# Performance work log

Hardware: AMD Instinct MI355X
Metric: run time of the kernel (lower is better)

The kernel has to match this reference:

```python
import jax, jax.numpy as jnp
import numpy as np

G = 32      # num_groups
T = 5       # Newton-Schulz iterations
EPS = 1e-5


def setup_inputs() -> dict:
    key = jax.random.key(0)
    x = jax.random.normal(key, (64, 256, 56, 56), dtype=jnp.float32)
    weight = jnp.ones((1, 256, 1, 1), dtype=jnp.float32)
    bias = jnp.zeros((1, 256, 1, 1), dtype=jnp.float32)
    return {"x": x, "weight": weight, "bias": bias}


def reference(x, weight, bias):
    N, C, H, W = x.shape
    # group view: (N*C//G, G, H, W) -> (G, N*C//G, H, W) -> (G, m)
    xg = x.reshape(N * C // G, G, H, W)
    xg = jnp.transpose(xg, (1, 0, 2, 3)).reshape(G, -1)
    m = xg.shape[1]

    mean = jnp.mean(xg, axis=1, keepdims=True)           # (G, 1)
    xm = xg - mean                                       # (G, m)
    sigma = (xm @ xm.T) / m + EPS * jnp.eye(G, dtype=x.dtype)  # (G, G)

    trace_inv = 1.0 / jnp.trace(sigma)
    sigma_N = sigma * trace_inv

    # Newton-Schulz: P_{k+1} = 1.5*P_k - 0.5*P_k^3 @ sigma_N
    P = jnp.eye(G, dtype=x.dtype)
    for _ in range(T):
        P = 1.5 * P - 0.5 * (P @ P @ P) @ sigma_N
    wm = P * jnp.sqrt(trace_inv)                         # inverse sqrt of sigma

    y = wm @ xm                                          # (G, m)
    out = y.reshape(G, N * C // G, H, W)
    out = jnp.transpose(out, (1, 0, 2, 3)).reshape(N, C, H, W)
    return out * weight + bias
```

## Files before the change

kernel.cpp:

```cpp
#include <hip/hip_runtime.h>


#define EPS 1e-5f
#define NS_ITERS 5
#define HW_ 3136
#define PANELS 512
#define PANEL_STRIDE 100352
#define M_COLS 1605632.0f
#define TPP 49
#define TILES_TOTAL 25088
#define NB1 512

#define WS_GRAM 0
#define WS_SUM 1024
#define WS_WMT 1056
#define WS_SHIFT 2080

typedef __attribute__((ext_vector_type(4))) float f32x4;
typedef __attribute__((ext_vector_type(8))) short short8v;

__device__ __forceinline__ unsigned f2bf2(float a, float b) {
  unsigned ua = __float_as_uint(a); ua = (ua + 0x7FFFu + ((ua >> 16) & 1u)) >> 16;
  unsigned ub = __float_as_uint(b); ub = (ub + 0x7FFFu + ((ub >> 16) & 1u)) >> 16;
  return ua | (ub << 16);
}

__device__ __forceinline__ int swzbyte(int r, int slotq) {
  const int ph = (((slotq) ^ (r & 7)) + 2 * (r >> 3)) & 7;
  return r * 128 + ph * 16;
}

__global__ __launch_bounds__(256) void k_stats(const float* __restrict__ x,
                                               float* __restrict__ ws) {
  __shared__ __align__(16) float smem[2048];
  unsigned short* tile = (unsigned short*)smem;
  const int tid = threadIdx.x;
  const int row_w = tid >> 4;
  const int c4 = tid & 15;
  const int pos = c4 << 2;
  const int wv = tid >> 6;
  const int lane = tid & 63;

  const int wa_lo = swzbyte(row_w, pos >> 3) + (pos & 7) * 2;
  const int wa_hi = swzbyte(row_w + 16, pos >> 3) + (pos & 7) * 2;

  const int fr_r = lane & 15;
  const int fr_sq = (wv >> 1) * 4 + (lane >> 4);
  const int ra0 = swzbyte(fr_r, fr_sq);
  const int ra1 = swzbyte(fr_r + 16, fr_sq);
  const bool bsel = (wv & 1);

  f32x4 acc0 = {0.f, 0.f, 0.f, 0.f};
  f32x4 acc1 = {0.f, 0.f, 0.f, 0.f};
  float sum_lo = 0.f, sum_hi = 0.f;

  for (int t = blockIdx.x; t < TILES_TOTAL; t += gridDim.x) {
    const int panel = t / TPP;
    const int tin = t - panel * TPP;
    const unsigned base = (unsigned)panel * PANEL_STRIDE + ((unsigned)tin << 6);
    const float4 v0 = *(const float4*)(x + base + row_w * HW_ + pos);
    const float4 v1 = *(const float4*)(x + base + (row_w + 16) * HW_ + pos);
    __syncthreads();
    *(uint2*)((char*)tile + wa_lo) = make_uint2(f2bf2(v0.x, v0.y), f2bf2(v0.z, v0.w));
    *(uint2*)((char*)tile + wa_hi) = make_uint2(f2bf2(v1.x, v1.y), f2bf2(v1.z, v1.w));
    sum_lo += v0.x + v0.y + v0.z + v0.w;
    sum_hi += v1.x + v1.y + v1.z + v1.w;
    __syncthreads();
    const short8v f0 = *(const short8v*)((char*)tile + ra0);
    const short8v f1 = *(const short8v*)((char*)tile + ra1);
    const short8v fB = bsel ? f1 : f0;
    acc0 = __builtin_amdgcn_mfma_f32_16x16x32_bf16(f0, fB, acc0, 0, 0, 0);
    acc1 = __builtin_amdgcn_mfma_f32_16x16x32_bf16(f1, fB, acc1, 0, 0, 0);
  }

  __syncthreads();
  {
    float* dst = smem + wv * 512 + lane * 8;
#pragma unroll
    for (int r = 0; r < 4; ++r) { dst[r] = acc0[r]; dst[4 + r] = acc1[r]; }
  }
  __syncthreads();
#pragma unroll
  for (int q = 0; q < 4; ++q) {
    const int e = q * 256 + tid;
    const int R = e >> 5, C = e & 31;
    const int cbh = C >> 4;
    const int ln = (((R & 15) >> 2) << 4) | (C & 15);
    const int idx = ((R >> 4) << 2) | (R & 3);
    const float s = smem[cbh * 512 + ln * 8 + idx] + smem[(cbh + 2) * 512 + ln * 8 + idx];
    atomicAdd(ws + WS_GRAM + e, s);
  }

  __syncthreads();
  smem[tid] = sum_lo;
  smem[256 + tid] = sum_hi;
  __syncthreads();
  if (tid < 32) {
    const int base2 = (tid < 16) ? tid * 16 : 256 + (tid - 16) * 16;
    float s = 0.f;
#pragma unroll
    for (int k = 0; k < 16; ++k) s += smem[base2 + k];
    atomicAdd(ws + WS_SUM + tid, s);
  }
}

__device__ __forceinline__ void mm32(float* __restrict__ D, const float* __restrict__ A,
                                     const float* __restrict__ B, int i, int cbase) {
  f32x4 a0 = {0.f,0.f,0.f,0.f}, a1 = a0, a2 = a0, a3 = a0;
#pragma unroll
  for (int k = 0; k < 32; ++k) {
    const float av = A[i * 36 + k];
    const float4 b0 = *(const float4*)(B + k * 36 + cbase);
    const float4 b1 = *(const float4*)(B + k * 36 + cbase + 4);
    const float4 b2 = *(const float4*)(B + k * 36 + cbase + 8);
    const float4 b3 = *(const float4*)(B + k * 36 + cbase + 12);
    a0[0] += av * b0.x; a0[1] += av * b0.y; a0[2] += av * b0.z; a0[3] += av * b0.w;
    a1[0] += av * b1.x; a1[1] += av * b1.y; a1[2] += av * b1.z; a1[3] += av * b1.w;
    a2[0] += av * b2.x; a2[1] += av * b2.y; a2[2] += av * b2.z; a2[3] += av * b2.w;
    a3[0] += av * b3.x; a3[1] += av * b3.y; a3[2] += av * b3.z; a3[3] += av * b3.w;
  }
  float* d = D + i * 36 + cbase;
#pragma unroll
  for (int r = 0; r < 4; ++r) { d[r] = a0[r]; d[4 + r] = a1[r]; d[8 + r] = a2[r]; d[12 + r] = a3[r]; }
}

__global__ __launch_bounds__(64) void k_ns(float* __restrict__ ws,
                                           const float* __restrict__ weight,
                                           const float* __restrict__ bias) {
  __shared__ float P[32 * 36], S[32 * 36], T1[32 * 36], T2[32 * 36];
  __shared__ float mean[32], msv[64], misc[1];
  const int lane = threadIdx.x;
  const int i = lane & 31;
  const int cbase = (lane >> 5) * 16;
  const float inv_m = 1.0f / M_COLS;

  if (lane < 32) mean[lane] = ws[WS_SUM + lane] * inv_m;
  __syncthreads();
#pragma unroll
  for (int q = 0; q < 16; ++q) {
    const int e = q * 64 + lane;
    const int R = e >> 5, C = e & 31;
    S[R * 36 + C] = ws[WS_GRAM + e] * inv_m - mean[R] * mean[C] + ((R == C) ? EPS : 0.f);
  }
  __syncthreads();
  if (lane == 0) {
    float tr = 0.f;
#pragma unroll
    for (int k = 0; k < 32; ++k) tr += S[k * 36 + k];
    misc[0] = 1.0f / tr;
  }
  __syncthreads();
  const float tinv = misc[0];
#pragma unroll
  for (int q = 0; q < 16; ++q) {
    const int e = q * 64 + lane;
    const int R = e >> 5, C = e & 31;
    S[R * 36 + C] *= tinv;
    P[R * 36 + C] = (R == C) ? 1.f : 0.f;
  }
  __syncthreads();

  for (int it = 0; it < NS_ITERS; ++it) {
    mm32(T1, P, P, i, cbase);
    __syncthreads();
    mm32(T2, T1, P, i, cbase);
    __syncthreads();
    mm32(T1, T2, S, i, cbase);
    __syncthreads();
#pragma unroll
    for (int cc = 0; cc < 16; ++cc) {
      const int c = cbase + cc;
      P[i * 36 + c] = 1.5f * P[i * 36 + c] - 0.5f * T1[i * 36 + c];
    }
    __syncthreads();
  }

  const float sq = sqrtf(tinv);
  float part = 0.f;
#pragma unroll
  for (int cc = 0; cc < 16; ++cc) {
    const int c = cbase + cc;
    const float wmv = P[i * 36 + c] * sq;
    ws[WS_WMT + c * 32 + i] = wmv;
    part += wmv * mean[c];
  }
  msv[lane] = part;
  __syncthreads();
#pragma unroll
  for (int q = 0; q < 4; ++q) {
    const int c = q * 64 + lane;
    const float m2 = msv[c & 31] + msv[32 + (c & 31)];
    ws[WS_SHIFT + c] = bias[c] - weight[c] * m2;
  }
}

__global__ __launch_bounds__(256, 4) void k_apply(const float* __restrict__ x,
                                                  const float* __restrict__ weight,
                                                  const float* __restrict__ ws,
                                                  float* __restrict__ out) {
  __shared__ float wmT[1024];
  __shared__ float wt[256], sh[256];
  const int tid = threadIdx.x;
  *(float4*)(wmT + tid * 4) = *(const float4*)(ws + WS_WMT + tid * 4);
  wt[tid] = weight[tid];
  sh[tid] = ws[WS_SHIFT + tid];
  __syncthreads();

  const unsigned J = blockIdx.x * 512u + (unsigned)tid * 2u;
  const unsigned panel = J / HW_;
  const unsigned p = J - panel * HW_;
  const unsigned base = panel * PANEL_STRIDE + p;
  const int cb = (int)(panel & 7u) * 32;

  float2 acc[32];
#pragma unroll
  for (int g = 0; g < 32; ++g) { acc[g].x = 0.f; acc[g].y = 0.f; }

#pragma unroll 4
  for (int gp = 0; gp < 32; ++gp) {
    const float2 v = *(const float2*)(x + base + gp * HW_);
#pragma unroll
    for (int g4 = 0; g4 < 8; ++g4) {
      const float4 w = *(const float4*)(wmT + gp * 32 + g4 * 4);
      acc[g4 * 4 + 0].x += w.x * v.x; acc[g4 * 4 + 0].y += w.x * v.y;
      acc[g4 * 4 + 1].x += w.y * v.x; acc[g4 * 4 + 1].y += w.y * v.y;
      acc[g4 * 4 + 2].x += w.z * v.x; acc[g4 * 4 + 2].y += w.z * v.y;
      acc[g4 * 4 + 3].x += w.w * v.x; acc[g4 * 4 + 3].y += w.w * v.y;
    }
  }

#pragma unroll
  for (int g = 0; g < 32; ++g) {
    const int c = cb + g;
    float2 o;
    o.x = acc[g].x * wt[c] + sh[c];
    o.y = acc[g].y * wt[c] + sh[c];
    *(float2*)(out + base + g * HW_) = o;
  }
}

extern "C" void kernel_launch(void* const* d_in, const int* in_sizes, int n_in,
                              void* d_out, int out_size, void* d_ws, size_t ws_size,
                              hipStream_t stream) {
  const float* x = (const float*)d_in[0];
  const float* w = (const float*)d_in[1];
  const float* b = (const float*)d_in[2];
  float* out = (float*)d_out;
  float* ws = (float*)d_ws;

  hipMemsetAsync(d_ws, 0, (1024 + 32) * sizeof(float), stream);
  hipLaunchKernelGGL(k_stats, dim3(NB1), dim3(256), 0, stream, x, ws);
  hipLaunchKernelGGL(k_ns, dim3(1), dim3(64), 0, stream, ws, w, b);
  hipLaunchKernelGGL(k_apply, dim3(3136), dim3(256), 0, stream, x, w, ws, out);
}
```

Measured before the change: 417.0 us.

## Replace atomic Gram reduction with per-block partials and a reduce kernel; widen NS

The stats kernel now writes each block's 32x32 Gram partial and its group sums to a private workspace slot instead of using global atomics. A new two-level reduction kernel sums them, which also removes the memset launch. The stats grid is doubled to 1024 blocks and the Newton-Schulz kernel is widened to 128 threads, each computing 8 columns. The apply kernel unrolls deeper and uses nontemporal stores for the output. The cost is one extra kernel launch and extra workspace traffic for the partials.

```diff
diff --git a/kernel.cpp b/kernel.cpp
--- a/kernel.cpp
+++ b/kernel.cpp
@@ -9,14 +9,17 @@
 #define M_COLS 1605632.0f
 #define TPP 49
 #define TILES_TOTAL 25088
-#define NB1 512
+#define NB1 1024
 
 #define WS_GRAM 0
 #define WS_SUM 1024
 #define WS_WMT 1056
 #define WS_SHIFT 2080
+#define WS_PART2 4096
+#define WS_PART 16384
 
 typedef __attribute__((ext_vector_type(4))) float f32x4;
+typedef __attribute__((ext_vector_type(2))) float f32x2v;
 typedef __attribute__((ext_vector_type(8))) short short8v;
 
 __device__ __forceinline__ unsigned f2bf2(float a, float b) {
@@ -80,6 +83,7 @@
     for (int r = 0; r < 4; ++r) { dst[r] = acc0[r]; dst[4 + r] = acc1[r]; }
   }
   __syncthreads();
+  float* part = ws + WS_PART + (unsigned)blockIdx.x * 1056u;
 #pragma unroll
   for (int q = 0; q < 4; ++q) {
     const int e = q * 256 + tid;
@@ -87,8 +91,7 @@
     const int cbh = C >> 4;
     const int ln = (((R & 15) >> 2) << 4) | (C & 15);
     const int idx = ((R >> 4) << 2) | (R & 3);
-    const float s = smem[cbh * 512 + ln * 8 + idx] + smem[(cbh + 2) * 512 + ln * 8 + idx];
-    atomicAdd(ws + WS_GRAM + e, s);
+    part[e] = smem[cbh * 512 + ln * 8 + idx] + smem[(cbh + 2) * 512 + ln * 8 + idx];
   }
 
   __syncthreads();
@@ -100,50 +103,65 @@
     float s = 0.f;
 #pragma unroll
     for (int k = 0; k < 16; ++k) s += smem[base2 + k];
-    atomicAdd(ws + WS_SUM + tid, s);
-  }
+    part[1024 + tid] = s;
+  }
+}
+
+__global__ __launch_bounds__(256) void k_reduce(float* __restrict__ ws) {
+  const int gid = blockIdx.x * 256 + threadIdx.x;
+  const int chunk = gid / 1056;
+  const int e = gid - chunk * 1056;
+  const float* src = ws + WS_PART + e + (unsigned)chunk * 128u * 1056u;
+  float s = 0.f;
+#pragma unroll 8
+  for (int b = 0; b < 128; ++b) s += src[(unsigned)b * 1056u];
+  ws[WS_PART2 + chunk * 1056 + e] = s;
 }
 
 __device__ __forceinline__ void mm32(float* __restrict__ D, const float* __restrict__ A,
                                      const float* __restrict__ B, int i, int cbase) {
-  f32x4 a0 = {0.f,0.f,0.f,0.f}, a1 = a0, a2 = a0, a3 = a0;
+  float a0[4] = {0.f, 0.f, 0.f, 0.f}, a1[4] = {0.f, 0.f, 0.f, 0.f};
 #pragma unroll
   for (int k = 0; k < 32; ++k) {
     const float av = A[i * 36 + k];
     const float4 b0 = *(const float4*)(B + k * 36 + cbase);
     const float4 b1 = *(const float4*)(B + k * 36 + cbase + 4);
-    const float4 b2 = *(const float4*)(B + k * 36 + cbase + 8);
-    const float4 b3 = *(const float4*)(B + k * 36 + cbase + 12);
     a0[0] += av * b0.x; a0[1] += av * b0.y; a0[2] += av * b0.z; a0[3] += av * b0.w;
     a1[0] += av * b1.x; a1[1] += av * b1.y; a1[2] += av * b1.z; a1[3] += av * b1.w;
-    a2[0] += av * b2.x; a2[1] += av * b2.y; a2[2] += av * b2.z; a2[3] += av * b2.w;
-    a3[0] += av * b3.x; a3[1] += av * b3.y; a3[2] += av * b3.z; a3[3] += av * b3.w;
   }
   float* d = D + i * 36 + cbase;
 #pragma unroll
-  for (int r = 0; r < 4; ++r) { d[r] = a0[r]; d[4 + r] = a1[r]; d[8 + r] = a2[r]; d[12 + r] = a3[r]; }
-}
-
-__global__ __launch_bounds__(64) void k_ns(float* __restrict__ ws,
-                                           const float* __restrict__ weight,
-                                           const float* __restrict__ bias) {
+  for (int r = 0; r < 4; ++r) { d[r] = a0[r]; d[4 + r] = a1[r]; }
+}
+
+__global__ __launch_bounds__(128) void k_ns(float* __restrict__ ws,
+                                            const float* __restrict__ weight,
+                                            const float* __restrict__ bias) {
   __shared__ float P[32 * 36], S[32 * 36], T1[32 * 36], T2[32 * 36];
-  __shared__ float mean[32], msv[64], misc[1];
-  const int lane = threadIdx.x;
-  const int i = lane & 31;
-  const int cbase = (lane >> 5) * 16;
+  __shared__ float mean[32], msv[128], misc[1];
+  const int tid = threadIdx.x;
+  const int i = tid & 31;
+  const int cbase = (tid >> 5) * 8;
   const float inv_m = 1.0f / M_COLS;
 
-  if (lane < 32) mean[lane] = ws[WS_SUM + lane] * inv_m;
-  __syncthreads();
-#pragma unroll
-  for (int q = 0; q < 16; ++q) {
-    const int e = q * 64 + lane;
+  if (tid < 32) {
+    float s = 0.f;
+#pragma unroll
+    for (int c = 0; c < 8; ++c) s += ws[WS_PART2 + c * 1056 + 1024 + tid];
+    mean[tid] = s * inv_m;
+  }
+  __syncthreads();
+#pragma unroll
+  for (int q = 0; q < 8; ++q) {
+    const int e = q * 128 + tid;
+    float s = 0.f;
+#pragma unroll
+    for (int c = 0; c < 8; ++c) s += ws[WS_PART2 + c * 1056 + e];
     const int R = e >> 5, C = e & 31;
-    S[R * 36 + C] = ws[WS_GRAM + e] * inv_m - mean[R] * mean[C] + ((R == C) ? EPS : 0.f);
-  }
-  __syncthreads();
-  if (lane == 0) {
+    S[R * 36 + C] = s * inv_m - mean[R] * mean[C] + ((R == C) ? EPS : 0.f);
+  }
+  __syncthreads();
+  if (tid == 0) {
     float tr = 0.f;
 #pragma unroll
     for (int k = 0; k < 32; ++k) tr += S[k * 36 + k];
@@ -152,8 +170,8 @@
   __syncthreads();
   const float tinv = misc[0];
 #pragma unroll
-  for (int q = 0; q < 16; ++q) {
-    const int e = q * 64 + lane;
+  for (int q = 0; q < 8; ++q) {
+    const int e = q * 128 + tid;
     const int R = e >> 5, C = e & 31;
     S[R * 36 + C] *= tinv;
     P[R * 36 + C] = (R == C) ? 1.f : 0.f;
@@ -168,7 +186,7 @@
     mm32(T1, T2, S, i, cbase);
     __syncthreads();
 #pragma unroll
-    for (int cc = 0; cc < 16; ++cc) {
+    for (int cc = 0; cc < 8; ++cc) {
       const int c = cbase + cc;
       P[i * 36 + c] = 1.5f * P[i * 36 + c] - 0.5f * T1[i * 36 + c];
     }
@@ -176,20 +194,21 @@
   }
 
   const float sq = sqrtf(tinv);
-  float part = 0.f;
-#pragma unroll
-  for (int cc = 0; cc < 16; ++cc) {
+  float partd = 0.f;
+#pragma unroll
+  for (int cc = 0; cc < 8; ++cc) {
     const int c = cbase + cc;
     const float wmv = P[i * 36 + c] * sq;
     ws[WS_WMT + c * 32 + i] = wmv;
-    part += wmv * mean[c];
-  }
-  msv[lane] = part;
-  __syncthreads();
-#pragma unroll
-  for (int q = 0; q < 4; ++q) {
-    const int c = q * 64 + lane;
-    const float m2 = msv[c & 31] + msv[32 + (c & 31)];
+    partd += wmv * mean[c];
+  }
+  msv[tid] = partd;
+  __syncthreads();
+#pragma unroll
+  for (int q = 0; q < 2; ++q) {
+    const int c = q * 128 + tid;
+    const int g = c & 31;
+    const float m2 = msv[g] + msv[32 + g] + msv[64 + g] + msv[96 + g];
     ws[WS_SHIFT + c] = bias[c] - weight[c] * m2;
   }
 }
@@ -216,7 +235,7 @@
 #pragma unroll
   for (int g = 0; g < 32; ++g) { acc[g].x = 0.f; acc[g].y = 0.f; }
 
-#pragma unroll 4
+#pragma unroll 8
   for (int gp = 0; gp < 32; ++gp) {
     const float2 v = *(const float2*)(x + base + gp * HW_);
 #pragma unroll
@@ -232,10 +251,10 @@
 #pragma unroll
   for (int g = 0; g < 32; ++g) {
     const int c = cb + g;
-    float2 o;
+    f32x2v o;
     o.x = acc[g].x * wt[c] + sh[c];
     o.y = acc[g].y * wt[c] + sh[c];
-    *(float2*)(out + base + g * HW_) = o;
+    __builtin_nontemporal_store(o, (f32x2v*)(out + base + g * HW_));
   }
 }
 
@@ -248,8 +267,8 @@
   float* out = (float*)d_out;
   float* ws = (float*)d_ws;
 
-  hipMemsetAsync(d_ws, 0, (1024 + 32) * sizeof(float), stream);
   hipLaunchKernelGGL(k_stats, dim3(NB1), dim3(256), 0, stream, x, ws);
-  hipLaunchKernelGGL(k_ns, dim3(1), dim3(64), 0, stream, ws, w, b);
+  hipLaunchKernelGGL(k_reduce, dim3(33), dim3(256), 0, stream, ws);
+  hipLaunchKernelGGL(k_ns, dim3(1), dim3(128), 0, stream, ws, w, b);
   hipLaunchKernelGGL(k_apply, dim3(3136), dim3(256), 0, stream, x, w, ws, out);
 }
```

Result: faster. 399.1 us (-4.3%).
